# Kernel optimization log

Measured on AMD Instinct MI355X. Metric: run time of the kernel, lower is better.

## Reference

```python
import jax, jax.numpy as jnp
import numpy as np

H = 16
D_K = 64
HALF_WINDOW = 256  # window_size // 2 = 512 // 2


def setup_inputs() -> dict:
    key = jax.random.key(0)
    ks = jax.random.split(key, 9)
    B, S, D = 2, 2048, 1024
    scale = 0.02
    return {
        "x": jax.random.normal(ks[0], (B, S, D), dtype=jnp.float32),
        "Wq": jax.random.normal(ks[1], (D, D), dtype=jnp.float32) * scale,
        "bq": jax.random.normal(ks[2], (D,), dtype=jnp.float32) * scale,
        "Wk": jax.random.normal(ks[3], (D, D), dtype=jnp.float32) * scale,
        "bk": jax.random.normal(ks[4], (D,), dtype=jnp.float32) * scale,
        "Wv": jax.random.normal(ks[5], (D, D), dtype=jnp.float32) * scale,
        "bv": jax.random.normal(ks[6], (D,), dtype=jnp.float32) * scale,
        "Wo": jax.random.normal(ks[7], (D, D), dtype=jnp.float32) * scale,
        "bo": jax.random.normal(ks[8], (D,), dtype=jnp.float32) * scale,
    }


def reference(x, Wq, bq, Wk, bk, Wv, bv, Wo, bo):
    B, S, D = x.shape
    # projections -> [B, H, S, d_k]
    q = (x @ Wq + bq).reshape(B, S, H, D_K).transpose(0, 2, 1, 3)
    k = (x @ Wk + bk).reshape(B, S, H, D_K).transpose(0, 2, 1, 3)
    v = (x @ Wv + bv).reshape(B, S, H, D_K).transpose(0, 2, 1, 3)
    # dense scores, as in the original module
    scores = jnp.einsum("bhqd,bhkd->bhqk", q, k) / jnp.sqrt(jnp.float32(D_K))
    # sliding window band mask: 0 inside |i-j| <= half_window, -inf outside
    idx = jnp.arange(S)
    band = jnp.abs(idx[:, None] - idx[None, :]) <= HALF_WINDOW  # [S, S]
    window_mask = jnp.where(band, jnp.float32(0.0), -jnp.inf)
    scores = scores + window_mask[None, None, :, :]
    attn = jax.nn.softmax(scores, axis=-1)  # dropout is identity (p=0 / eval)
    out = jnp.einsum("bhqk,bhkd->bhqd", attn, v)  # [B, H, S, d_k]
    out = out.transpose(0, 2, 1, 3).reshape(B, S, D)
    return out @ Wo + bo
```

## Files before the change

kernel.cpp:

```cpp
#include <hip/hip_runtime.h>
#include <hip/hip_bf16.h>
#include <cstdint>
#include <cstddef>

using bf16 = __hip_bfloat16;
typedef __attribute__((ext_vector_type(8))) short bf16x8v;
typedef __attribute__((ext_vector_type(4))) float f32x4v;
typedef __attribute__((ext_vector_type(16))) float f32x16v;
typedef __attribute__((ext_vector_type(4))) int i32x4v;

__device__ __forceinline__ f32x4v mfma16x16x32(bf16x8v a, bf16x8v b, f32x4v c) {
  return __builtin_amdgcn_mfma_f32_16x16x32_bf16(a, b, c, 0, 0, 0);
}
__device__ __forceinline__ f32x16v mfma32x32x16(bf16x8v a, bf16x8v b, f32x16v c) {
  return __builtin_amdgcn_mfma_f32_32x32x16_bf16(a, b, c, 0, 0, 0);
}

__device__ __forceinline__ void lds_async16(const void* g, void* l) {
  __builtin_amdgcn_global_load_lds(
      (__attribute__((address_space(1))) void*)g,
      (__attribute__((address_space(3))) void*)l, 16, 0, 0);
}

__device__ __forceinline__ unsigned short f2bf_bits(float f) {
  union { bf16 h; unsigned short u; } cv;
  cv.h = __float2bfloat16(f);
  return cv.u;
}
__device__ __forceinline__ uint32_t pk_bf2(float a, float b) {
  return (uint32_t)f2bf_bits(a) | ((uint32_t)f2bf_bits(b) << 16);
}

#define QSC 0.18033688011111793f


__global__ void convert_x_k(const float* __restrict__ x, bf16* __restrict__ xb) {
  const int i = blockIdx.x * blockDim.x + threadIdx.x;
  const float4 v = reinterpret_cast<const float4*>(x)[i];
  ushort4 o;
  o.x = f2bf_bits(v.x); o.y = f2bf_bits(v.y);
  o.z = f2bf_bits(v.z); o.w = f2bf_bits(v.w);
  reinterpret_cast<ushort4*>(xb)[i] = o;
}

__global__ void transpose_w_k(const float* __restrict__ Wq, const float* __restrict__ Wk,
                              const float* __restrict__ Wv, const float* __restrict__ Wo,
                              bf16* __restrict__ wcat, bf16* __restrict__ wot) {
  __shared__ float tile[64][65];
  const int mat = blockIdx.z;
  const float* W = (mat == 0) ? Wq : (mat == 1) ? Wk : (mat == 2) ? Wv : Wo;
  bf16* dst = (mat < 3) ? (wcat + (size_t)mat * 1024 * 1024) : wot;
  const int n0 = blockIdx.x * 64, k0 = blockIdx.y * 64;
  const int tr = threadIdx.x >> 6, tc = threadIdx.x & 63;
#pragma unroll
  for (int it = 0; it < 16; ++it)
    tile[it * 4 + tr][tc] = W[(size_t)(k0 + it * 4 + tr) * 1024 + n0 + tc];
  __syncthreads();
#pragma unroll
  for (int it = 0; it < 16; ++it) {
    const int n = n0 + it * 4 + tr;
    dst[(size_t)n * 1024 + k0 + tc] = __float2bfloat16(tile[tc][it * 4 + tr]);
  }
}

__global__ void build_bias_k(const float* __restrict__ bq, const float* __restrict__ bk,
                             const float* __restrict__ bv, float* __restrict__ bcat) {
  const int i = blockIdx.x * 256 + threadIdx.x;
  if (i < 3072)
    bcat[i] = (i < 1024) ? bq[i] : (i < 2048) ? bk[i - 1024] : bv[i - 2048];
}

template <int EPI>
__global__ __launch_bounds__(256, 3) void gemm_k(
    const bf16* __restrict__ A, const bf16* __restrict__ Bt,
    const float* __restrict__ bias,
    bf16* __restrict__ qb, bf16* __restrict__ kb, bf16* __restrict__ vtb,
    float* __restrict__ outf)
{
  constexpr int K = 1024;
  __shared__ bf16 smem[16384];
  const int t = threadIdx.x;
  const int lane = t & 63, w = t >> 6;
  const int g = lane >> 4, r = lane & 15;
  const int wr = w >> 1, wc = w & 1;
  const int m0 = blockIdx.x * 128, n0 = blockIdx.y * 128;

  const int srow = t >> 2;
  const int scol = ((lane & 3) ^ g) << 3;
  const bf16* aS0 = A + (size_t)(m0 + srow) * K + scol;
  const bf16* aS1 = A + (size_t)(m0 + 64 + srow) * K + scol;
  const bf16* bS0 = Bt + (size_t)(n0 + srow) * K + scol;
  const bf16* bS1 = Bt + (size_t)(n0 + 64 + srow) * K + scol;

  f32x4v acc[4][4] = {};

  auto STAGE = [&](int kt, int buf) {
    const int ko = kt * 32;
    char* d0 = (char*)smem + buf * 16384 + w * 1024;
    lds_async16(aS0 + ko, d0);
    lds_async16(aS1 + ko, d0 + 4096);
    lds_async16(bS0 + ko, d0 + 8192);
    lds_async16(bS1 + ko, d0 + 12288);
  };

  const int csw = (g ^ ((r >> 2) & 3)) << 4;

  STAGE(0, 0);
  asm volatile("s_waitcnt vmcnt(0)" ::: "memory");
  __builtin_amdgcn_s_barrier();

  for (int kt = 0; kt < 32; ++kt) {
    if (kt < 31) STAGE(kt + 1, (kt + 1) & 1);

    const char* buf = (const char*)smem + (kt & 1) * 16384;
    bf16x8v af[4], bfr[4];
#pragma unroll
    for (int m = 0; m < 4; ++m)
      af[m] = *reinterpret_cast<const bf16x8v*>(buf + (wr * 64 + m * 16 + r) * 64 + csw);
#pragma unroll
    for (int n = 0; n < 4; ++n)
      bfr[n] = *reinterpret_cast<const bf16x8v*>(buf + 8192 + (wc * 64 + n * 16 + r) * 64 + csw);
#pragma unroll
    for (int m = 0; m < 4; ++m)
#pragma unroll
      for (int n = 0; n < 4; ++n)
        acc[m][n] = mfma16x16x32(af[m], bfr[n], acc[m][n]);

    if (kt < 31) asm volatile("s_waitcnt vmcnt(0)" ::: "memory");
    __builtin_amdgcn_s_barrier();
  }

  if (EPI == 0) {
    const int gcol0 = n0 + wc * 64;
    const int mat = gcol0 >> 10;
    const int hh = (gcol0 & 1023) >> 6;
    const int s0 = m0 + wr * 64;
    const int b_ = s0 >> 11, sb = s0 & 2047;
    const size_t bh = (size_t)(b_ * 16 + hh);
    unsigned short* ep = (unsigned short*)smem + w * 4096;

#pragma unroll
    for (int n = 0; n < 4; ++n) {
      const int dkl = n * 16 + r;
      const float bv_ = bias[gcol0 + dkl];
#pragma unroll
      for (int m = 0; m < 4; ++m) {
#pragma unroll
        for (int v = 0; v < 4; ++v) {
          const int sl = m * 16 + g * 4 + v;
          const float val = acc[m][n][v] + bv_;
          if (mat == 0)      ep[sl * 64 + dkl] = f2bf_bits(val * QSC);
          else if (mat == 1) ep[sl * 64 + dkl] = f2bf_bits(val);
          else               ep[dkl * 64 + sl] = f2bf_bits(val);
        }
      }
    }
#pragma unroll
    for (int i = 0; i < 8; ++i) {
      const int chunk = i * 64 + lane;
      const int rw = chunk >> 3;
      const int off = (chunk & 7) * 8;
      const bf16x8v vv = *reinterpret_cast<const bf16x8v*>(ep + rw * 64 + off);
      if (mat == 0)
        *reinterpret_cast<bf16x8v*>(qb + (bh * 2048 + sb + rw) * 64 + off) = vv;
      else if (mat == 1)
        *reinterpret_cast<bf16x8v*>(kb + (bh * 2048 + sb + rw) * 64 + off) = vv;
      else
        *reinterpret_cast<bf16x8v*>(vtb + (bh * 64 + rw) * 2048 + sb + off) = vv;
    }
  } else {
#pragma unroll
    for (int n = 0; n < 4; ++n) {
      const int gcol = n0 + wc * 64 + n * 16 + r;
      const float bv_ = bias[gcol];
#pragma unroll
      for (int m = 0; m < 4; ++m) {
#pragma unroll
        for (int v = 0; v < 4; ++v) {
          const int grow = m0 + wr * 64 + m * 16 + g * 4 + v;
          outf[(size_t)grow * 1024 + gcol] = acc[m][n][v] + bv_;
        }
      }
    }
  }
}

__global__ __launch_bounds__(64) void attn_k(
    const bf16* __restrict__ qb, const bf16* __restrict__ kb_,
    const bf16* __restrict__ vtb, bf16* __restrict__ aout)
{
  constexpr int S = 2048;
  const int lane = threadIdx.x & 63;
  const int hi = lane >> 5, l31 = lane & 31;
  const int d_ = blockIdx.x;
  const int xcd = d_ & 7, slot = d_ >> 3;
  const int bh_i = xcd * 4 + (slot >> 6);
  const int q0 = (slot & 63) * 32;
  const int b = bh_i >> 4, h = bh_i & 15;
  const size_t bh = (size_t)b * 16 + h;
  const bf16* qp = qb + bh * (size_t)(S * 64);
  const bf16* kp = kb_ + bh * (size_t)(S * 64);
  const bf16* vp = vtb + bh * (size_t)(64 * S);

  bf16x8v qf[4];
#pragma unroll
  for (int i = 0; i < 4; ++i)
    qf[i] = *reinterpret_cast<const bf16x8v*>(&qp[(size_t)(q0 + l31) * 64 + i * 16 + hi * 8]);

  f32x16v o0 = {}, o1 = {};
  float lrun = 0.f;

  const int jlo = (q0 >= 256) ? (q0 - 256) : 0;
  const int jend = (q0 + 256 <= S - 32) ? (q0 + 256) : (S - 32);
  const int nIter = ((jend - jlo) >> 5) + 1;

  auto LDK = [&](int j, bf16x8v* kf) {
    const bf16* p0 = kp + (size_t)(j + l31) * 64 + hi * 8;
#pragma unroll
    for (int i = 0; i < 4; ++i)
      kf[i] = *reinterpret_cast<const bf16x8v*>(p0 + i * 16);
  };
  auto LDV = [&](int j, bf16x8v* vf) {
#pragma unroll
    for (int db = 0; db < 2; ++db)
#pragma unroll
      for (int kk = 0; kk < 2; ++kk)
        vf[db * 2 + kk] = *reinterpret_cast<const bf16x8v*>(
            &vp[(size_t)(db * 32 + l31) * S + j + kk * 16 + hi * 8]);
  };

  auto STEP = [&](int idx, bf16x8v* kc, bf16x8v* vc, bf16x8v* kn, bf16x8v* vn) {
    const int j = jlo + idx * 32;
    if (idx + 1 < nIter) { LDK(j + 32, kn); LDV(j + 32, vn); }

    f32x16v s = {};
#pragma unroll
    for (int i = 0; i < 4; ++i) s = mfma32x32x16(kc[i], qf[i], s);

    float p[16];
    const bool needMask = ((q0 + 31 - j) > 256) || ((j + 31 - q0) > 256);
    if (needMask) {
      const int base = l31 - 4 * hi + (q0 - j) + 256;
#pragma unroll
      for (int tt = 0; tt < 4; ++tt)
#pragma unroll
        for (int e = 0; e < 4; ++e) {
          const int kk_ = 8 * tt + e;
          const float ev = __builtin_amdgcn_exp2f(s[4 * tt + e]);
          p[4 * tt + e] = ((unsigned)(base - kk_) <= 512u) ? ev : 0.f;
        }
    } else {
#pragma unroll
      for (int i = 0; i < 16; ++i) p[i] = __builtin_amdgcn_exp2f(s[i]);
    }
    lrun += (((p[0] + p[1]) + (p[2] + p[3])) + ((p[4] + p[5]) + (p[6] + p[7]))) +
            (((p[8] + p[9]) + (p[10] + p[11])) + ((p[12] + p[13]) + (p[14] + p[15])));

    uint32_t W00 = pk_bf2(p[0],  p[1]),  W01 = pk_bf2(p[2],  p[3]);
    uint32_t W10 = pk_bf2(p[4],  p[5]),  W11 = pk_bf2(p[6],  p[7]);
    uint32_t W20 = pk_bf2(p[8],  p[9]),  W21 = pk_bf2(p[10], p[11]);
    uint32_t W30 = pk_bf2(p[12], p[13]), W31 = pk_bf2(p[14], p[15]);
    asm volatile("v_permlane32_swap_b32 %0, %1" : "+v"(W00), "+v"(W10));
    asm volatile("v_permlane32_swap_b32 %0, %1" : "+v"(W01), "+v"(W11));
    asm volatile("v_permlane32_swap_b32 %0, %1" : "+v"(W20), "+v"(W30));
    asm volatile("v_permlane32_swap_b32 %0, %1" : "+v"(W21), "+v"(W31));
    union { i32x4v i; bf16x8v hv; } c0, c1;
    c0.i = (i32x4v){(int)W00, (int)W01, (int)W10, (int)W11};
    c1.i = (i32x4v){(int)W20, (int)W21, (int)W30, (int)W31};
    o0 = mfma32x32x16(vc[0], c0.hv, o0);
    o0 = mfma32x32x16(vc[1], c1.hv, o0);
    o1 = mfma32x32x16(vc[2], c0.hv, o1);
    o1 = mfma32x32x16(vc[3], c1.hv, o1);
  };

  bf16x8v ka[4], va[4], kn2[4], vn2[4];
  LDK(jlo, ka); LDV(jlo, va);
  int it = 0;
  while (it + 2 <= nIter) {
    STEP(it, ka, va, kn2, vn2);
    STEP(it + 1, kn2, vn2, ka, va);
    it += 2;
  }
  if (it < nIter) STEP(it, ka, va, kn2, vn2);

  lrun += __shfl_xor(lrun, 32);
  const float inv = 1.0f / lrun;

  const size_t ob = ((size_t)b * S + q0 + l31) * 1024 + h * 64 + hi * 4;
#pragma unroll
  for (int tt = 0; tt < 4; ++tt) {
    uint2 u;
    u.x = pk_bf2(o0[4 * tt] * inv, o0[4 * tt + 1] * inv);
    u.y = pk_bf2(o0[4 * tt + 2] * inv, o0[4 * tt + 3] * inv);
    *reinterpret_cast<uint2*>(&aout[ob + 8 * tt]) = u;
    uint2 v2;
    v2.x = pk_bf2(o1[4 * tt] * inv, o1[4 * tt + 1] * inv);
    v2.y = pk_bf2(o1[4 * tt + 2] * inv, o1[4 * tt + 3] * inv);
    *reinterpret_cast<uint2*>(&aout[ob + 32 + 8 * tt]) = v2;
  }
}

extern "C" void kernel_launch(void* const* d_in, const int* in_sizes, int n_in,
                              void* d_out, int out_size, void* d_ws, size_t ws_size,
                              hipStream_t stream) {
  (void)in_sizes; (void)n_in; (void)out_size; (void)ws_size;
  const float* x  = (const float*)d_in[0];
  const float* Wq = (const float*)d_in[1];
  const float* bq = (const float*)d_in[2];
  const float* Wk = (const float*)d_in[3];
  const float* bk = (const float*)d_in[4];
  const float* Wv = (const float*)d_in[5];
  const float* bv = (const float*)d_in[6];
  const float* Wo = (const float*)d_in[7];
  const float* bo = (const float*)d_in[8];
  float* out = (float*)d_out;

  char* ws = (char*)d_ws;
  bf16*  xb    = (bf16*)(ws);
  bf16*  wcat  = (bf16*)(ws + 8388608);
  bf16*  wot   = (bf16*)(ws + 14680064);
  bf16*  qbuf  = (bf16*)(ws + 16777216);
  bf16*  kbuf  = (bf16*)(ws + 25165824);
  bf16*  vtbuf = (bf16*)(ws + 33554432);
  bf16*  aoutb = (bf16*)(ws + 41943040);
  float* bcat  = (float*)(ws + 50331648);

  convert_x_k<<<4096, 256, 0, stream>>>(x, xb);
  transpose_w_k<<<dim3(16, 16, 4), 256, 0, stream>>>(Wq, Wk, Wv, Wo, wcat, wot);
  build_bias_k<<<12, 256, 0, stream>>>(bq, bk, bv, bcat);

  gemm_k<0><<<dim3(32, 24), 256, 0, stream>>>(xb, wcat, bcat, qbuf, kbuf, vtbuf, nullptr);
  attn_k<<<2048, 64, 0, stream>>>(qbuf, kbuf, vtbuf, aoutb);
  gemm_k<1><<<dim3(32, 8), 256, 0, stream>>>(aoutb, wot, bo, nullptr, nullptr, nullptr, out);
}
```

Measured before the change: 105.4 us.

## Fuse prep kernels, load GEMM A operand directly to registers, remap workgroups

Merges the x conversion, weight transpose and bias build into one prep launch to save launch overhead. The GEMM now stages only the B tile through LDS and loads A fragments straight from global memory into registers with a software double buffer, which halves LDS traffic and footprint. A one-dimensional grid with an XCD-aware workgroup remap is meant to improve L2 locality. The epilogue staging is split into two halves to fit the smaller LDS buffer. Uncoalesced direct A loads from global memory may cost more bandwidth than they save.

```diff
diff --git a/kernel.cpp b/kernel.cpp
--- a/kernel.cpp
+++ b/kernel.cpp
@@ -33,41 +33,44 @@
 
 #define QSC 0.18033688011111793f
 
-
-__global__ void convert_x_k(const float* __restrict__ x, bf16* __restrict__ xb) {
-  const int i = blockIdx.x * blockDim.x + threadIdx.x;
-  const float4 v = reinterpret_cast<const float4*>(x)[i];
-  ushort4 o;
-  o.x = f2bf_bits(v.x); o.y = f2bf_bits(v.y);
-  o.z = f2bf_bits(v.z); o.w = f2bf_bits(v.w);
-  reinterpret_cast<ushort4*>(xb)[i] = o;
-}
-
-__global__ void transpose_w_k(const float* __restrict__ Wq, const float* __restrict__ Wk,
-                              const float* __restrict__ Wv, const float* __restrict__ Wo,
-                              bf16* __restrict__ wcat, bf16* __restrict__ wot) {
+__global__ void prep_k(const float* __restrict__ x,
+                       const float* __restrict__ Wq, const float* __restrict__ Wk,
+                       const float* __restrict__ Wv, const float* __restrict__ Wo,
+                       const float* __restrict__ bq, const float* __restrict__ bk,
+                       const float* __restrict__ bv,
+                       bf16* __restrict__ xb, bf16* __restrict__ wcat,
+                       bf16* __restrict__ wot, float* __restrict__ bcat)
+{
   __shared__ float tile[64][65];
-  const int mat = blockIdx.z;
-  const float* W = (mat == 0) ? Wq : (mat == 1) ? Wk : (mat == 2) ? Wv : Wo;
-  bf16* dst = (mat < 3) ? (wcat + (size_t)mat * 1024 * 1024) : wot;
-  const int n0 = blockIdx.x * 64, k0 = blockIdx.y * 64;
-  const int tr = threadIdx.x >> 6, tc = threadIdx.x & 63;
-#pragma unroll
-  for (int it = 0; it < 16; ++it)
-    tile[it * 4 + tr][tc] = W[(size_t)(k0 + it * 4 + tr) * 1024 + n0 + tc];
-  __syncthreads();
-#pragma unroll
-  for (int it = 0; it < 16; ++it) {
-    const int n = n0 + it * 4 + tr;
-    dst[(size_t)n * 1024 + k0 + tc] = __float2bfloat16(tile[tc][it * 4 + tr]);
-  }
-}
-
-__global__ void build_bias_k(const float* __restrict__ bq, const float* __restrict__ bk,
-                             const float* __restrict__ bv, float* __restrict__ bcat) {
-  const int i = blockIdx.x * 256 + threadIdx.x;
-  if (i < 3072)
-    bcat[i] = (i < 1024) ? bq[i] : (i < 2048) ? bk[i - 1024] : bv[i - 2048];
+  const int bid = blockIdx.x;
+  if (bid < 4096) {
+    const int i = bid * 256 + threadIdx.x;
+    const float4 v = reinterpret_cast<const float4*>(x)[i];
+    ushort4 o;
+    o.x = f2bf_bits(v.x); o.y = f2bf_bits(v.y);
+    o.z = f2bf_bits(v.z); o.w = f2bf_bits(v.w);
+    reinterpret_cast<ushort4*>(xb)[i] = o;
+  } else if (bid < 5120) {
+    const int b2 = bid - 4096;
+    const int mat = b2 >> 8;
+    const float* W = (mat == 0) ? Wq : (mat == 1) ? Wk : (mat == 2) ? Wv : Wo;
+    bf16* dst = (mat < 3) ? (wcat + (size_t)mat * 1024 * 1024) : wot;
+    const int n0 = ((b2 >> 4) & 15) * 64, k0 = (b2 & 15) * 64;
+    const int tr = threadIdx.x >> 6, tc = threadIdx.x & 63;
+#pragma unroll
+    for (int it = 0; it < 16; ++it)
+      tile[it * 4 + tr][tc] = W[(size_t)(k0 + it * 4 + tr) * 1024 + n0 + tc];
+    __syncthreads();
+#pragma unroll
+    for (int it = 0; it < 16; ++it) {
+      const int n = n0 + it * 4 + tr;
+      dst[(size_t)n * 1024 + k0 + tc] = __float2bfloat16(tile[tc][it * 4 + tr]);
+    }
+  } else {
+    const int i = (bid - 5120) * 256 + threadIdx.x;
+    if (i < 3072)
+      bcat[i] = (i < 1024) ? bq[i] : (i < 2048) ? bk[i - 1024] : bv[i - 2048];
+  }
 }
 
 template <int EPI>
@@ -78,95 +81,115 @@
     float* __restrict__ outf)
 {
   constexpr int K = 1024;
-  __shared__ bf16 smem[16384];
+  constexpr int NT = (EPI == 0) ? 24 : 8;
+  constexpr int NWG = (EPI == 0) ? 768 : 256;
+  __shared__ bf16 Bs[2][128 * 32];
   const int t = threadIdx.x;
   const int lane = t & 63, w = t >> 6;
   const int g = lane >> 4, r = lane & 15;
   const int wr = w >> 1, wc = w & 1;
-  const int m0 = blockIdx.x * 128, n0 = blockIdx.y * 128;
-
-  const int srow = t >> 2;
-  const int scol = ((lane & 3) ^ g) << 3;
-  const bf16* aS0 = A + (size_t)(m0 + srow) * K + scol;
-  const bf16* aS1 = A + (size_t)(m0 + 64 + srow) * K + scol;
-  const bf16* bS0 = Bt + (size_t)(n0 + srow) * K + scol;
-  const bf16* bS1 = Bt + (size_t)(n0 + 64 + srow) * K + scol;
+
+  const int dd = blockIdx.x;
+  const int wg = (dd & 7) * (NWG / 8) + (dd >> 3);
+  const int m0 = (wg / NT) * 128, n0 = (wg % NT) * 128;
+
+  const bf16* bS0 = Bt + (size_t)(n0 + (t >> 2)) * K + (lane & 3) * 8;
+  const bf16* bS1 = bS0 + (size_t)64 * K;
+
+  const bf16* aP = A + (size_t)(m0 + wr * 64 + r) * K + g * 8;
 
   f32x4v acc[4][4] = {};
-
-  auto STAGE = [&](int kt, int buf) {
-    const int ko = kt * 32;
-    char* d0 = (char*)smem + buf * 16384 + w * 1024;
-    lds_async16(aS0 + ko, d0);
-    lds_async16(aS1 + ko, d0 + 4096);
-    lds_async16(bS0 + ko, d0 + 8192);
-    lds_async16(bS1 + ko, d0 + 12288);
-  };
-
-  const int csw = (g ^ ((r >> 2) & 3)) << 4;
-
-  STAGE(0, 0);
+  bf16x8v aCur[4], aNxt[4];
+
+  auto STAGEB = [&](int kt, int buf) {
+    char* d = (char*)&Bs[buf][0] + w * 1024;
+    lds_async16(bS0 + kt * 32, d);
+    lds_async16(bS1 + kt * 32, d + 4096);
+  };
+  auto LDA = [&](int kt, bf16x8v* a) {
+#pragma unroll
+    for (int m = 0; m < 4; ++m)
+      a[m] = *reinterpret_cast<const bf16x8v*>(aP + (size_t)m * 16 * K + kt * 32);
+  };
+  auto COMPUTE = [&](const bf16* bp, bf16x8v* af) {
+    bf16x8v bf_[4];
+#pragma unroll
+    for (int n = 0; n < 4; ++n)
+      bf_[n] = *reinterpret_cast<const bf16x8v*>(
+          (const char*)bp + (wc * 64 + n * 16 + r) * 64 + g * 16);
+#pragma unroll
+    for (int m = 0; m < 4; ++m)
+#pragma unroll
+      for (int n = 0; n < 4; ++n)
+        acc[m][n] = mfma16x16x32(af[m], bf_[n], acc[m][n]);
+  };
+
+  STAGEB(0, 0);
+  LDA(0, aCur);
   asm volatile("s_waitcnt vmcnt(0)" ::: "memory");
   __builtin_amdgcn_s_barrier();
 
-  for (int kt = 0; kt < 32; ++kt) {
-    if (kt < 31) STAGE(kt + 1, (kt + 1) & 1);
-
-    const char* buf = (const char*)smem + (kt & 1) * 16384;
-    bf16x8v af[4], bfr[4];
-#pragma unroll
-    for (int m = 0; m < 4; ++m)
-      af[m] = *reinterpret_cast<const bf16x8v*>(buf + (wr * 64 + m * 16 + r) * 64 + csw);
-#pragma unroll
-    for (int n = 0; n < 4; ++n)
-      bfr[n] = *reinterpret_cast<const bf16x8v*>(buf + 8192 + (wc * 64 + n * 16 + r) * 64 + csw);
-#pragma unroll
-    for (int m = 0; m < 4; ++m)
-#pragma unroll
-      for (int n = 0; n < 4; ++n)
-        acc[m][n] = mfma16x16x32(af[m], bfr[n], acc[m][n]);
-
-    if (kt < 31) asm volatile("s_waitcnt vmcnt(0)" ::: "memory");
+  for (int k2 = 0; k2 < 16; ++k2) {
+    const int kt = 2 * k2;
+    STAGEB(kt + 1, 1);
+    LDA(kt + 1, aNxt);
+    COMPUTE(&Bs[0][0], aCur);
+    asm volatile("s_waitcnt vmcnt(0)" ::: "memory");
     __builtin_amdgcn_s_barrier();
+    if (k2 < 15) {
+      STAGEB(kt + 2, 0);
+      LDA(kt + 2, aCur);
+    }
+    COMPUTE(&Bs[1][0], aNxt);
+    if (k2 < 15) asm volatile("s_waitcnt vmcnt(0)" ::: "memory");
+    __builtin_amdgcn_s_barrier();
   }
 
   if (EPI == 0) {
-    const int gcol0 = n0 + wc * 64;
-    const int mat = gcol0 >> 10;
-    const int hh = (gcol0 & 1023) >> 6;
+    const int gc0 = n0 + wc * 64;
+    const int mat = gc0 >> 10;
+    const int hh = (gc0 & 1023) >> 6;
     const int s0 = m0 + wr * 64;
     const int b_ = s0 >> 11, sb = s0 & 2047;
     const size_t bh = (size_t)(b_ * 16 + hh);
-    unsigned short* ep = (unsigned short*)smem + w * 4096;
-
-#pragma unroll
-    for (int n = 0; n < 4; ++n) {
-      const int dkl = n * 16 + r;
-      const float bv_ = bias[gcol0 + dkl];
-#pragma unroll
-      for (int m = 0; m < 4; ++m) {
-#pragma unroll
-        for (int v = 0; v < 4; ++v) {
-          const int sl = m * 16 + g * 4 + v;
-          const float val = acc[m][n][v] + bv_;
-          if (mat == 0)      ep[sl * 64 + dkl] = f2bf_bits(val * QSC);
-          else if (mat == 1) ep[sl * 64 + dkl] = f2bf_bits(val);
-          else               ep[dkl * 64 + sl] = f2bf_bits(val);
+    unsigned short* ep = (unsigned short*)&Bs[0][0] + w * 2048;
+
+#pragma unroll
+    for (int h = 0; h < 2; ++h) {
+#pragma unroll
+      for (int nn = 0; nn < 2; ++nn) {
+        const int n = 2 * h + nn;
+        const int dkl = nn * 16 + r;
+        const float bv_ = bias[gc0 + h * 32 + dkl];
+#pragma unroll
+        for (int m = 0; m < 4; ++m)
+#pragma unroll
+          for (int v = 0; v < 4; ++v) {
+            const int sl = m * 16 + g * 4 + v;
+            const float val = acc[m][n][v] + bv_;
+            if (mat == 0)      ep[sl * 32 + dkl] = f2bf_bits(val * QSC);
+            else if (mat == 1) ep[sl * 32 + dkl] = f2bf_bits(val);
+            else               ep[dkl * 64 + sl] = f2bf_bits(val);
+          }
+      }
+      if (mat < 2) {
+        bf16* dst = (mat == 0) ? qb : kb;
+#pragma unroll
+        for (int i = 0; i < 4; ++i) {
+          const int c = i * 64 + lane;
+          const int row = c >> 2, cg = c & 3;
+          const bf16x8v vv = *reinterpret_cast<const bf16x8v*>(ep + row * 32 + cg * 8);
+          *reinterpret_cast<bf16x8v*>(dst + (bh * 2048 + sb + row) * 64 + h * 32 + cg * 8) = vv;
+        }
+      } else {
+#pragma unroll
+        for (int i = 0; i < 4; ++i) {
+          const int c = i * 64 + lane;
+          const int row = c >> 3, cg = c & 7;
+          const bf16x8v vv = *reinterpret_cast<const bf16x8v*>(ep + row * 64 + cg * 8);
+          *reinterpret_cast<bf16x8v*>(vtb + (bh * 64 + h * 32 + row) * 2048 + sb + cg * 8) = vv;
         }
       }
-    }
-#pragma unroll
-    for (int i = 0; i < 8; ++i) {
-      const int chunk = i * 64 + lane;
-      const int rw = chunk >> 3;
-      const int off = (chunk & 7) * 8;
-      const bf16x8v vv = *reinterpret_cast<const bf16x8v*>(ep + rw * 64 + off);
-      if (mat == 0)
-        *reinterpret_cast<bf16x8v*>(qb + (bh * 2048 + sb + rw) * 64 + off) = vv;
-      else if (mat == 1)
-        *reinterpret_cast<bf16x8v*>(kb + (bh * 2048 + sb + rw) * 64 + off) = vv;
-      else
-        *reinterpret_cast<bf16x8v*>(vtb + (bh * 64 + rw) * 2048 + sb + off) = vv;
     }
   } else {
 #pragma unroll
@@ -325,11 +348,10 @@
   bf16*  aoutb = (bf16*)(ws + 41943040);
   float* bcat  = (float*)(ws + 50331648);
 
-  convert_x_k<<<4096, 256, 0, stream>>>(x, xb);
-  transpose_w_k<<<dim3(16, 16, 4), 256, 0, stream>>>(Wq, Wk, Wv, Wo, wcat, wot);
-  build_bias_k<<<12, 256, 0, stream>>>(bq, bk, bv, bcat);
-
-  gemm_k<0><<<dim3(32, 24), 256, 0, stream>>>(xb, wcat, bcat, qbuf, kbuf, vtbuf, nullptr);
+  prep_k<<<5132, 256, 0, stream>>>(x, Wq, Wk, Wv, Wo, bq, bk, bv,
+                                   xb, wcat, wot, bcat);
+
+  gemm_k<0><<<768, 256, 0, stream>>>(xb, wcat, bcat, qbuf, kbuf, vtbuf, nullptr);
   attn_k<<<2048, 64, 0, stream>>>(qbuf, kbuf, vtbuf, aoutb);
-  gemm_k<1><<<dim3(32, 8), 256, 0, stream>>>(aoutb, wot, bo, nullptr, nullptr, nullptr, out);
-}
+  gemm_k<1><<<256, 256, 0, stream>>>(aoutb, wot, bo, nullptr, nullptr, nullptr, out);
+}
```

Measured after the change: 142.2 us. +34.9%, slower.
